# Optimization experiments

Measured on AMD Instinct MI355X. Metric: run time of the kernel, lower is better.

Reference implementation:

```python
import jax, jax.numpy as jnp
import numpy as np

NUM_HEADS = 16

def setup_inputs() -> dict:
    key = jax.random.key(0)
    kq, kk, kv = jax.random.split(key, 3)
    B, S, E = 4, 2048, 1024
    Q = jax.random.normal(kq, (B, S, E), dtype=jnp.float32)
    K = jax.random.normal(kk, (B, S, E), dtype=jnp.float32)
    V = jax.random.normal(kv, (B, S, E), dtype=jnp.float32)
    return {"Q": Q, "K": K, "V": V}

def reference(Q, K, V):
    B, S, E = Q.shape
    H = NUM_HEADS
    d_k = E // H
    # [B, H, S, d_k]
    q = Q.reshape(B, S, H, d_k).transpose(0, 2, 1, 3)
    k = K.reshape(B, S, H, d_k).transpose(0, 2, 1, 3)
    v = V.reshape(B, S, H, d_k).transpose(0, 2, 1, 3)
    scale = 1.0 / np.sqrt(d_k).astype(np.float32)
    # [B, H, S, S] full score matrix (naive attention, as in the original)
    scores = jnp.einsum('bhqd,bhkd->bhqk', q, k) * scale
    causal_mask = jnp.tril(jnp.ones((S, S), dtype=bool))
    scores = jnp.where(causal_mask, scores, jnp.finfo(scores.dtype).min)
    attn = jax.nn.softmax(scores, axis=-1)
    out = jnp.einsum('bhqk,bhkd->bhqd', attn, v)
    return out.transpose(0, 2, 1, 3).reshape(B, S, E)
```

## Files before the change

### kernel.cpp

```cpp
#include <hip/hip_runtime.h>
#include <hip/hip_bf16.h>

namespace {

constexpr int NUM_HEADS = 16;
constexpr int DK   = 64;
constexpr int SEQ  = 2048;
constexpr int EMB  = 1024;
constexpr int BR   = 128;
constexpr int BC   = 64;
constexpr int PSTR = 76;
constexpr int TILE_BYTES = 64 * 64 * 2;
constexpr float QSCALE = 0.18033688011112042f;

using frag_ab = __attribute__((ext_vector_type(8))) short;
using frag_cd = __attribute__((ext_vector_type(4))) float;

__device__ inline short f2bf(float f) {
  unsigned int u = __float_as_uint(f);
  u += 0x7fffu + ((u >> 16) & 1u);
  return (short)(u >> 16);
}

__device__ inline unsigned int pk_bf16(float a, float b) {
#if __has_builtin(__builtin_amdgcn_cvt_pk_bf16_f32)
  typedef __attribute__((ext_vector_type(2))) __bf16 bf16x2;
  bf16x2 r = __builtin_amdgcn_cvt_pk_bf16_f32(a, b);
  unsigned int u;
  __builtin_memcpy(&u, &r, 4);
  return u;
#else
  return (unsigned int)(unsigned short)f2bf(a) |
         ((unsigned int)(unsigned short)f2bf(b) << 16);
#endif
}

__device__ inline float fast_exp2(float x) {
#if __has_builtin(__builtin_amdgcn_exp2f)
  return __builtin_amdgcn_exp2f(x);
#else
  return exp2f(x);
#endif
}

__device__ __forceinline__ void gld_lds16(const void* gsrc, void* ldst) {
  __builtin_amdgcn_global_load_lds(
      (const __attribute__((address_space(1))) unsigned int*)gsrc,
      (__attribute__((address_space(3))) unsigned int*)ldst, 16, 0, 0);
}

__global__ __launch_bounds__(256)
void fa_prep(const float* __restrict__ K, const float* __restrict__ V,
             char* __restrict__ Kw, char* __restrict__ Vw)
{
  const int tid  = threadIdx.x;
  const int bh   = blockIdx.x >> 5;
  const int tile = blockIdx.x & 31;
  const int b = bh / NUM_HEADS, h = bh % NUM_HEADS;
  const float* Kb = K + (size_t)b * SEQ * EMB + h * DK;
  const float* Vb = V + (size_t)b * SEQ * EMB + h * DK;
  char* kt = Kw + ((size_t)bh * 32 + tile) * TILE_BYTES;
  char* vt = Vw + ((size_t)bh * 32 + tile) * TILE_BYTES;

#pragma unroll
  for (int i = 0; i < 2; ++i) {
    const int w = tid + i * 256;
    const int row = w >> 3, cd = w & 7;
    const float* src = Kb + (size_t)(tile * 64 + row) * EMB + cd * 8;
    const float4 a  = *(const float4*)src;
    const float4 b4 = *(const float4*)(src + 4);
    uint4 o;
    o.x = pk_bf16(a.x, a.y);  o.y = pk_bf16(a.z, a.w);
    o.z = pk_bf16(b4.x, b4.y); o.w = pk_bf16(b4.z, b4.w);
    *(uint4*)(kt + row * 128 + ((cd ^ (row & 7)) * 16)) = o;
  }
#pragma unroll
  for (int i = 0; i < 2; ++i) {
    const int w = tid + i * 256;
    const int d = w & 63, kc = w >> 6;
    float v[8];
#pragma unroll
    for (int j = 0; j < 8; ++j)
      v[j] = Vb[(size_t)(tile * 64 + kc * 8 + j) * EMB + d];
    uint4 o;
    o.x = pk_bf16(v[0], v[1]); o.y = pk_bf16(v[2], v[3]);
    o.z = pk_bf16(v[4], v[5]); o.w = pk_bf16(v[6], v[7]);
    *(uint4*)(vt + d * 128 + ((kc ^ (d & 7)) * 16)) = o;
  }
}

__global__ __launch_bounds__(256)
void fa_fwd(const float* __restrict__ Q, const char* __restrict__ Kw,
            const char* __restrict__ Vw, float* __restrict__ O)
{
  const int tid  = threadIdx.x;
  const int wave = tid >> 6;
  const int lane = tid & 63;
  const int m    = lane & 15;
  const int quad = lane >> 4;
  const int mm7  = m & 7;

  constexpr int numQ  = SEQ / BR;
  constexpr int pairs = numQ / 2;
  const int bh = blockIdx.x / pairs;
  const int p  = blockIdx.x % pairs;
  const int b  = bh / NUM_HEADS;
  const int h  = bh % NUM_HEADS;

  const float* Qb = Q + (size_t)b * SEQ * EMB + h * DK;
  float*       Ob = O + (size_t)b * SEQ * EMB + h * DK;
  const char* KwT = Kw + (size_t)bh * 32 * TILE_BYTES;
  const char* VwT = Vw + (size_t)bh * 32 * TILE_BYTES;

  __shared__ __align__(16) short Kl[64 * 64];
  __shared__ __align__(16) short Vt[64 * 64];
  __shared__ __align__(16) float Pf[4][16 * PSTR];

  const char* sbase = (wave < 2 ? KwT : VwT);
  short*      dbase = (wave < 2 ? Kl : Vt) + (wave & 1) * 2048;
  const int   shalf = (wave & 1) * 4096;

  frag_ab ones;
#pragma unroll
  for (int j = 0; j < 8; ++j) ones[j] = (short)0x3F80;

  for (int t = 0; t < 2; ++t) {
    const int qt = t ? p : (numQ - 1 - p);
    const int q0 = qt * BR;
    const int row0w = q0 + wave * 32;

    frag_ab qf[2][2];
#pragma unroll
    for (int mt = 0; mt < 2; ++mt) {
      const int qrow = row0w + mt * 16 + m;
      const float* qp = Qb + (size_t)qrow * EMB + quad * 8;
#pragma unroll
      for (int c = 0; c < 2; ++c) {
        const float4 a  = *(const float4*)(qp + c * 32);
        const float4 b4 = *(const float4*)(qp + c * 32 + 4);
        union { frag_ab f; unsigned int u[4]; } pk;
        pk.u[0] = pk_bf16(a.x * QSCALE, a.y * QSCALE);
        pk.u[1] = pk_bf16(a.z * QSCALE, a.w * QSCALE);
        pk.u[2] = pk_bf16(b4.x * QSCALE, b4.y * QSCALE);
        pk.u[3] = pk_bf16(b4.z * QSCALE, b4.w * QSCALE);
        qf[mt][c] = pk.f;
      }
    }

    frag_cd acc_o[2][4];
    frag_cd acc_l[2];
#pragma unroll
    for (int mt = 0; mt < 2; ++mt) {
      acc_l[mt] = frag_cd{0.f, 0.f, 0.f, 0.f};
#pragma unroll
      for (int n = 0; n < 4; ++n) acc_o[mt][n] = frag_cd{0.f, 0.f, 0.f, 0.f};
    }

    const int nIter = 2 * (qt + 1);
    for (int it = 0; it < nIter; ++it) {
      const int kbase = it * BC;

      __syncthreads();
      {
        const char* src = sbase + (size_t)it * TILE_BYTES + shalf + lane * 16;
#pragma unroll
        for (int j = 0; j < 4; ++j)
          gld_lds16(src + j * 1024, (char*)dbase + j * 1024);
      }
      __syncthreads();

      frag_cd s[2][4];
#pragma unroll
      for (int mt = 0; mt < 2; ++mt)
#pragma unroll
        for (int n = 0; n < 4; ++n) s[mt][n] = frag_cd{0.f, 0.f, 0.f, 0.f};
#pragma unroll
      for (int n = 0; n < 4; ++n) {
#pragma unroll
        for (int c = 0; c < 2; ++c) {
          frag_ab kf = *(const frag_ab*)(&Kl[(n * 16 + m) * 64 + (((c * 4 + quad) ^ mm7) * 8)]);
#pragma unroll
          for (int mt = 0; mt < 2; ++mt)
            s[mt][n] = __builtin_amdgcn_mfma_f32_16x16x32_bf16(qf[mt][c], kf, s[mt][n], 0, 0, 0);
        }
      }

#pragma unroll
      for (int mt = 0; mt < 2; ++mt) {
        const int row0 = row0w + mt * 16;
        if (kbase + BC > row0) {
#pragma unroll
          for (int n = 0; n < 4; ++n) {
            const int kcol = kbase + n * 16 + m;
#pragma unroll
            for (int r = 0; r < 4; ++r) {
              const int qr = row0 + quad * 4 + r;
              if (kcol > qr) s[mt][n][r] = -1e30f;
            }
          }
        }
      }

#pragma unroll
      for (int mt = 0; mt < 2; ++mt)
#pragma unroll
        for (int n = 0; n < 4; ++n)
#pragma unroll
          for (int r = 0; r < 4; ++r)
            s[mt][n][r] = fast_exp2(s[mt][n][r]);

      frag_ab vf[4][2];
#pragma unroll
      for (int n = 0; n < 4; ++n)
#pragma unroll
        for (int c = 0; c < 2; ++c)
          vf[n][c] = *(const frag_ab*)(&Vt[(n * 16 + m) * 64 + (((c * 4 + quad) ^ mm7) * 8)]);

#pragma unroll
      for (int mt = 0; mt < 2; ++mt) {
#pragma unroll
        for (int n = 0; n < 4; ++n)
#pragma unroll
          for (int r = 0; r < 4; ++r)
            Pf[wave][(quad * 4 + r) * PSTR + n * 16 + m] = s[mt][n][r];

#pragma unroll
        for (int c = 0; c < 2; ++c) {
          const float* pr = &Pf[wave][m * PSTR + c * 32 + quad * 8];
          const float4 p0 = *(const float4*)pr;
          const float4 p1 = *(const float4*)(pr + 4);
          union { frag_ab f; unsigned int u[4]; } pk;
          pk.u[0] = pk_bf16(p0.x, p0.y);
          pk.u[1] = pk_bf16(p0.z, p0.w);
          pk.u[2] = pk_bf16(p1.x, p1.y);
          pk.u[3] = pk_bf16(p1.z, p1.w);
#pragma unroll
          for (int n = 0; n < 4; ++n)
            acc_o[mt][n] = __builtin_amdgcn_mfma_f32_16x16x32_bf16(pk.f, vf[n][c], acc_o[mt][n], 0, 0, 0);
          acc_l[mt] = __builtin_amdgcn_mfma_f32_16x16x32_bf16(pk.f, ones, acc_l[mt], 0, 0, 0);
        }
      }
    }

#pragma unroll
    for (int mt = 0; mt < 2; ++mt)
#pragma unroll
      for (int r = 0; r < 4; ++r) {
        const float inv = 1.0f / acc_l[mt][r];
        const int qr = row0w + mt * 16 + quad * 4 + r;
        float* op = Ob + (size_t)qr * EMB;
#pragma unroll
        for (int n = 0; n < 4; ++n)
          op[n * 16 + m] = acc_o[mt][n][r] * inv;
      }
  }
}

__global__ __launch_bounds__(256)
void fa_fwd_fb(const float* __restrict__ Q, const float* __restrict__ K,
               const float* __restrict__ V, float* __restrict__ O)
{
  constexpr int FBR = 64, FBC = 64, FLSTR = 72;
  const int tid  = threadIdx.x;
  const int wave = tid >> 6;
  const int lane = tid & 63;
  const int m    = lane & 15;
  const int quad = lane >> 4;

  constexpr int numQ  = SEQ / FBR;
  constexpr int pairs = numQ / 2;
  const int bh = blockIdx.x / pairs;
  const int p  = blockIdx.x % pairs;
  const int b  = bh / NUM_HEADS;
  const int h  = bh % NUM_HEADS;

  const float* Qb = Q + (size_t)b * SEQ * EMB + h * DK;
  const float* Kb = K + (size_t)b * SEQ * EMB + h * DK;
  const float* Vb = V + (size_t)b * SEQ * EMB + h * DK;
  float*       Ob = O + (size_t)b * SEQ * EMB + h * DK;

  __shared__ __align__(16) short Kl[FBC * FLSTR];
  __shared__ __align__(16) short Vt[DK * FLSTR];
  __shared__ __align__(16) float Pf[4][16 * PSTR];

  for (int t = 0; t < 2; ++t) {
    const int qt = t ? p : (numQ - 1 - p);
    const int q0 = qt * FBR;

    frag_ab qf[2];
    {
      const int qrow = q0 + wave * 16 + m;
      const float* qp = Qb + (size_t)qrow * EMB + quad * 8;
#pragma unroll
      for (int c = 0; c < 2; ++c) {
        const float4 a  = *(const float4*)(qp + c * 32);
        const float4 b4 = *(const float4*)(qp + c * 32 + 4);
        union { frag_ab f; unsigned int u[4]; } pk;
        pk.u[0] = pk_bf16(a.x * QSCALE, a.y * QSCALE);
        pk.u[1] = pk_bf16(a.z * QSCALE, a.w * QSCALE);
        pk.u[2] = pk_bf16(b4.x * QSCALE, b4.y * QSCALE);
        pk.u[3] = pk_bf16(b4.z * QSCALE, b4.w * QSCALE);
        qf[c] = pk.f;
      }
    }

    float l_r[4] = {0.f, 0.f, 0.f, 0.f};
    frag_cd acc_o[4];
#pragma unroll
    for (int n = 0; n < 4; ++n) acc_o[n] = frag_cd{0.f, 0.f, 0.f, 0.f};

    const int nIter = qt + 1;
    for (int it = 0; it < nIter; ++it) {
      const int kbase = it * FBC;
      __syncthreads();
#pragma unroll
      for (int i = 0; i < 4; ++i) {
        const int idx = tid + i * 256;
        const int row = idx >> 4;
        const int c4  = (idx & 15) << 2;
        const float4 kv = *(const float4*)(Kb + (size_t)(kbase + row) * EMB + c4);
        uint2 ks;
        ks.x = pk_bf16(kv.x, kv.y);
        ks.y = pk_bf16(kv.z, kv.w);
        *(uint2*)(&Kl[row * FLSTR + c4]) = ks;
      }
#pragma unroll
      for (int i = 0; i < 2; ++i) {
        const int w    = tid + i * 256;
        const int rowp = w >> 4;
        const int c4   = (w & 15) << 2;
        const float* vp = Vb + (size_t)(kbase + 2 * rowp) * EMB + c4;
        const float4 v0 = *(const float4*)(vp);
        const float4 v1 = *(const float4*)(vp + EMB);
        *(unsigned int*)(&Vt[(c4 + 0) * FLSTR + 2 * rowp]) = pk_bf16(v0.x, v1.x);
        *(unsigned int*)(&Vt[(c4 + 1) * FLSTR + 2 * rowp]) = pk_bf16(v0.y, v1.y);
        *(unsigned int*)(&Vt[(c4 + 2) * FLSTR + 2 * rowp]) = pk_bf16(v0.z, v1.z);
        *(unsigned int*)(&Vt[(c4 + 3) * FLSTR + 2 * rowp]) = pk_bf16(v0.w, v1.w);
      }
      __syncthreads();

      frag_cd s[4];
#pragma unroll
      for (int n = 0; n < 4; ++n) {
        frag_cd a = frag_cd{0.f, 0.f, 0.f, 0.f};
#pragma unroll
        for (int c = 0; c < 2; ++c) {
          frag_ab kf = *(const frag_ab*)(&Kl[(n * 16 + m) * FLSTR + c * 32 + quad * 8]);
          a = __builtin_amdgcn_mfma_f32_16x16x32_bf16(qf[c], kf, a, 0, 0, 0);
        }
        s[n] = a;
      }
      if (kbase + FBC > q0) {
#pragma unroll
        for (int n = 0; n < 4; ++n) {
          const int kcol = kbase + n * 16 + m;
#pragma unroll
          for (int r = 0; r < 4; ++r) {
            const int qr = q0 + wave * 16 + quad * 4 + r;
            if (kcol > qr) s[n][r] = -1e30f;
          }
        }
      }
#pragma unroll
      for (int n = 0; n < 4; ++n)
#pragma unroll
        for (int r = 0; r < 4; ++r)
          s[n][r] = fast_exp2(s[n][r]);
#pragma unroll
      for (int r = 0; r < 4; ++r) {
        float rs = (s[0][r] + s[1][r]) + (s[2][r] + s[3][r]);
        rs += __shfl_xor(rs, 1);
        rs += __shfl_xor(rs, 2);
        rs += __shfl_xor(rs, 4);
        rs += __shfl_xor(rs, 8);
        l_r[r] += rs;
      }
#pragma unroll
      for (int n = 0; n < 4; ++n)
#pragma unroll
        for (int r = 0; r < 4; ++r)
          Pf[wave][(quad * 4 + r) * PSTR + n * 16 + m] = s[n][r];
#pragma unroll
      for (int c = 0; c < 2; ++c) {
        const float* pr = &Pf[wave][m * PSTR + c * 32 + quad * 8];
        const float4 p0 = *(const float4*)pr;
        const float4 p1 = *(const float4*)(pr + 4);
        union { frag_ab f; unsigned int u[4]; } pk;
        pk.u[0] = pk_bf16(p0.x, p0.y);
        pk.u[1] = pk_bf16(p0.z, p0.w);
        pk.u[2] = pk_bf16(p1.x, p1.y);
        pk.u[3] = pk_bf16(p1.z, p1.w);
#pragma unroll
        for (int n = 0; n < 4; ++n) {
          frag_ab vf = *(const frag_ab*)(&Vt[(n * 16 + m) * FLSTR + c * 32 + quad * 8]);
          acc_o[n] = __builtin_amdgcn_mfma_f32_16x16x32_bf16(pk.f, vf, acc_o[n], 0, 0, 0);
        }
      }
    }
#pragma unroll
    for (int r = 0; r < 4; ++r) {
      const float inv = 1.0f / l_r[r];
      const int qr = q0 + wave * 16 + quad * 4 + r;
      float* op = Ob + (size_t)qr * EMB;
#pragma unroll
      for (int n = 0; n < 4; ++n)
        op[n * 16 + m] = acc_o[n][r] * inv;
    }
  }
}

}

extern "C" void kernel_launch(void* const* d_in, const int* in_sizes, int n_in,
                              void* d_out, int out_size, void* d_ws, size_t ws_size,
                              hipStream_t stream) {
  const float* Q = (const float*)d_in[0];
  const float* K = (const float*)d_in[1];
  const float* V = (const float*)d_in[2];
  float* O = (float*)d_out;
  const int B = in_sizes[0] / (SEQ * EMB);
  const size_t kw_bytes = (size_t)B * NUM_HEADS * 32 * TILE_BYTES;

  if (ws_size >= 2 * kw_bytes) {
    char* Kw = (char*)d_ws;
    char* Vw = Kw + kw_bytes;
    fa_prep<<<B * NUM_HEADS * 32, 256, 0, stream>>>(K, V, Kw, Vw);
    fa_fwd<<<B * NUM_HEADS * (SEQ / BR / 2), 256, 0, stream>>>(Q, Kw, Vw, O);
  } else {
    fa_fwd_fb<<<B * NUM_HEADS * 16, 256, 0, stream>>>(Q, K, V, O);
  }
}
```

Baseline: 212.4 us.

## Double-buffer K/V tiles and launch one block per query tile

The kernel now keeps two LDS buffers for K and V and issues the async load of the next tile before computing on the current one, replacing two barriers per iteration with one. The paired-tile scheme, where each block handled a long and a short causal row block, is dropped. Instead there is one block per 128-row query tile, with heavy tiles scheduled first. Each wave also skips whole iterations that fall entirely above its causal diagonal. This doubles LDS usage and may reduce occupancy, and the grid doubles with unbalanced per-block work.

```diff
diff --git a/kernel.cpp b/kernel.cpp
--- a/kernel.cpp
+++ b/kernel.cpp
@@ -100,75 +100,81 @@
   const int quad = lane >> 4;
   const int mm7  = m & 7;
 
-  constexpr int numQ  = SEQ / BR;
-  constexpr int pairs = numQ / 2;
-  const int bh = blockIdx.x / pairs;
-  const int p  = blockIdx.x % pairs;
+  constexpr int numQ = SEQ / BR;
+  const int bh = blockIdx.x >> 4;
+  const int qt = (numQ - 1) - (blockIdx.x & 15);
   const int b  = bh / NUM_HEADS;
   const int h  = bh % NUM_HEADS;
+  const int q0 = qt * BR;
+  const int row0w = q0 + wave * 32;
 
   const float* Qb = Q + (size_t)b * SEQ * EMB + h * DK;
   float*       Ob = O + (size_t)b * SEQ * EMB + h * DK;
   const char* KwT = Kw + (size_t)bh * 32 * TILE_BYTES;
   const char* VwT = Vw + (size_t)bh * 32 * TILE_BYTES;
 
-  __shared__ __align__(16) short Kl[64 * 64];
-  __shared__ __align__(16) short Vt[64 * 64];
+  __shared__ __align__(16) short Kl[2][64 * 64];
+  __shared__ __align__(16) short Vt[2][64 * 64];
   __shared__ __align__(16) float Pf[4][16 * PSTR];
 
   const char* sbase = (wave < 2 ? KwT : VwT);
-  short*      dbase = (wave < 2 ? Kl : Vt) + (wave & 1) * 2048;
   const int   shalf = (wave & 1) * 4096;
 
   frag_ab ones;
 #pragma unroll
   for (int j = 0; j < 8; ++j) ones[j] = (short)0x3F80;
 
-  for (int t = 0; t < 2; ++t) {
-    const int qt = t ? p : (numQ - 1 - p);
-    const int q0 = qt * BR;
-    const int row0w = q0 + wave * 32;
-
-    frag_ab qf[2][2];
-#pragma unroll
-    for (int mt = 0; mt < 2; ++mt) {
-      const int qrow = row0w + mt * 16 + m;
-      const float* qp = Qb + (size_t)qrow * EMB + quad * 8;
-#pragma unroll
-      for (int c = 0; c < 2; ++c) {
-        const float4 a  = *(const float4*)(qp + c * 32);
-        const float4 b4 = *(const float4*)(qp + c * 32 + 4);
-        union { frag_ab f; unsigned int u[4]; } pk;
-        pk.u[0] = pk_bf16(a.x * QSCALE, a.y * QSCALE);
-        pk.u[1] = pk_bf16(a.z * QSCALE, a.w * QSCALE);
-        pk.u[2] = pk_bf16(b4.x * QSCALE, b4.y * QSCALE);
-        pk.u[3] = pk_bf16(b4.z * QSCALE, b4.w * QSCALE);
-        qf[mt][c] = pk.f;
-      }
-    }
-
-    frag_cd acc_o[2][4];
-    frag_cd acc_l[2];
-#pragma unroll
-    for (int mt = 0; mt < 2; ++mt) {
-      acc_l[mt] = frag_cd{0.f, 0.f, 0.f, 0.f};
-#pragma unroll
-      for (int n = 0; n < 4; ++n) acc_o[mt][n] = frag_cd{0.f, 0.f, 0.f, 0.f};
-    }
-
-    const int nIter = 2 * (qt + 1);
-    for (int it = 0; it < nIter; ++it) {
-      const int kbase = it * BC;
-
-      __syncthreads();
-      {
-        const char* src = sbase + (size_t)it * TILE_BYTES + shalf + lane * 16;
-#pragma unroll
-        for (int j = 0; j < 4; ++j)
-          gld_lds16(src + j * 1024, (char*)dbase + j * 1024);
-      }
-      __syncthreads();
-
+  frag_ab qf[2][2];
+#pragma unroll
+  for (int mt = 0; mt < 2; ++mt) {
+    const int qrow = row0w + mt * 16 + m;
+    const float* qp = Qb + (size_t)qrow * EMB + quad * 8;
+#pragma unroll
+    for (int c = 0; c < 2; ++c) {
+      const float4 a  = *(const float4*)(qp + c * 32);
+      const float4 b4 = *(const float4*)(qp + c * 32 + 4);
+      union { frag_ab f; unsigned int u[4]; } pk;
+      pk.u[0] = pk_bf16(a.x * QSCALE, a.y * QSCALE);
+      pk.u[1] = pk_bf16(a.z * QSCALE, a.w * QSCALE);
+      pk.u[2] = pk_bf16(b4.x * QSCALE, b4.y * QSCALE);
+      pk.u[3] = pk_bf16(b4.z * QSCALE, b4.w * QSCALE);
+      qf[mt][c] = pk.f;
+    }
+  }
+
+  frag_cd acc_o[2][4];
+  frag_cd acc_l[2];
+#pragma unroll
+  for (int mt = 0; mt < 2; ++mt) {
+    acc_l[mt] = frag_cd{0.f, 0.f, 0.f, 0.f};
+#pragma unroll
+    for (int n = 0; n < 4; ++n) acc_o[mt][n] = frag_cd{0.f, 0.f, 0.f, 0.f};
+  }
+
+  const int nIter = 2 * (qt + 1);
+
+  {
+    char* dst = (char*)(wave < 2 ? &Kl[0][0] : &Vt[0][0]) + shalf;
+    const char* src = sbase + shalf + lane * 16;
+#pragma unroll
+    for (int j = 0; j < 4; ++j)
+      gld_lds16(src + j * 1024, dst + j * 1024);
+  }
+  __syncthreads();
+
+  for (int it = 0; it < nIter; ++it) {
+    const int buf   = it & 1;
+    const int kbase = it * BC;
+
+    if (it + 1 < nIter) {
+      char* dst = (char*)(wave < 2 ? &Kl[buf ^ 1][0] : &Vt[buf ^ 1][0]) + shalf;
+      const char* src = sbase + (size_t)(it + 1) * TILE_BYTES + shalf + lane * 16;
+#pragma unroll
+      for (int j = 0; j < 4; ++j)
+        gld_lds16(src + j * 1024, dst + j * 1024);
+    }
+
+    if (kbase <= row0w + 31) {
       frag_cd s[2][4];
 #pragma unroll
       for (int mt = 0; mt < 2; ++mt)
@@ -178,7 +184,7 @@
       for (int n = 0; n < 4; ++n) {
 #pragma unroll
         for (int c = 0; c < 2; ++c) {
-          frag_ab kf = *(const frag_ab*)(&Kl[(n * 16 + m) * 64 + (((c * 4 + quad) ^ mm7) * 8)]);
+          frag_ab kf = *(const frag_ab*)(&Kl[buf][(n * 16 + m) * 64 + (((c * 4 + quad) ^ mm7) * 8)]);
 #pragma unroll
           for (int mt = 0; mt < 2; ++mt)
             s[mt][n] = __builtin_amdgcn_mfma_f32_16x16x32_bf16(qf[mt][c], kf, s[mt][n], 0, 0, 0);
@@ -214,7 +220,7 @@
       for (int n = 0; n < 4; ++n)
 #pragma unroll
         for (int c = 0; c < 2; ++c)
-          vf[n][c] = *(const frag_ab*)(&Vt[(n * 16 + m) * 64 + (((c * 4 + quad) ^ mm7) * 8)]);
+          vf[n][c] = *(const frag_ab*)(&Vt[buf][(n * 16 + m) * 64 + (((c * 4 + quad) ^ mm7) * 8)]);
 
 #pragma unroll
       for (int mt = 0; mt < 2; ++mt) {
@@ -242,18 +248,20 @@
       }
     }
 
-#pragma unroll
-    for (int mt = 0; mt < 2; ++mt)
-#pragma unroll
-      for (int r = 0; r < 4; ++r) {
-        const float inv = 1.0f / acc_l[mt][r];
-        const int qr = row0w + mt * 16 + quad * 4 + r;
-        float* op = Ob + (size_t)qr * EMB;
-#pragma unroll
-        for (int n = 0; n < 4; ++n)
-          op[n * 16 + m] = acc_o[mt][n][r] * inv;
-      }
-  }
+    __syncthreads();
+  }
+
+#pragma unroll
+  for (int mt = 0; mt < 2; ++mt)
+#pragma unroll
+    for (int r = 0; r < 4; ++r) {
+      const float inv = 1.0f / acc_l[mt][r];
+      const int qr = row0w + mt * 16 + quad * 4 + r;
+      float* op = Ob + (size_t)qr * EMB;
+#pragma unroll
+      for (int n = 0; n < 4; ++n)
+        op[n * 16 + m] = acc_o[mt][n][r] * inv;
+    }
 }
 
 __global__ __launch_bounds__(256)
@@ -425,7 +433,7 @@
     char* Kw = (char*)d_ws;
     char* Vw = Kw + kw_bytes;
     fa_prep<<<B * NUM_HEADS * 32, 256, 0, stream>>>(K, V, Kw, Vw);
-    fa_fwd<<<B * NUM_HEADS * (SEQ / BR / 2), 256, 0, stream>>>(Q, Kw, Vw, O);
+    fa_fwd<<<B * NUM_HEADS * (SEQ / BR), 256, 0, stream>>>(Q, Kw, Vw, O);
   } else {
     fa_fwd_fb<<<B * NUM_HEADS * 16, 256, 0, stream>>>(Q, K, V, O);
   }
```

Result: slower. 239.5 us (+12.8%).

## Split causal attention KV work evenly across blocks with partial-sum combine kernel

Applied to the files above, without the earlier changes.

Replaces the paired-query-tile forward kernel with a split-KV scheme. Each of 16 blocks per head processes exactly 17 of the 272 causal KV tile-steps, flattened across query tiles. Query tiles that straddle block boundaries write partial unnormalized outputs (bf16) and row sums to workspace, and a new combine kernel sums and normalizes them. It also skips fully masked KV tiles per wave, changes the P scratch stride, and sets an occupancy hint. This aims at load balance and double the block count, at the cost of an extra launch, extra workspace traffic, and bf16 rounding of partial accumulators.

```diff
diff --git a/kernel.cpp b/kernel.cpp
--- a/kernel.cpp
+++ b/kernel.cpp
@@ -9,8 +9,9 @@
 constexpr int EMB  = 1024;
 constexpr int BR   = 128;
 constexpr int BC   = 64;
-constexpr int PSTR = 76;
+constexpr int PSTR = 68;
 constexpr int TILE_BYTES = 64 * 64 * 2;
+constexpr int SLOT_BYTES = 128 * 64 * 2 + 128 * 4;
 constexpr float QSCALE = 0.18033688011112042f;
 
 using frag_ab = __attribute__((ext_vector_type(8))) short;
@@ -48,6 +49,8 @@
       (const __attribute__((address_space(1))) unsigned int*)gsrc,
       (__attribute__((address_space(3))) unsigned int*)ldst, 16, 0, 0);
 }
+
+__device__ __forceinline__ int tile_prefix(int qt) { return 270 - qt * qt - 3 * qt; }
 
 __global__ __launch_bounds__(256)
 void fa_prep(const float* __restrict__ K, const float* __restrict__ V,
@@ -89,9 +92,10 @@
   }
 }
 
-__global__ __launch_bounds__(256)
-void fa_fwd(const float* __restrict__ Q, const char* __restrict__ Kw,
-            const char* __restrict__ Vw, float* __restrict__ O)
+__global__ __launch_bounds__(256, 4)
+void fa_split(const float* __restrict__ Q, const char* __restrict__ Kw,
+              const char* __restrict__ Vw, float* __restrict__ O,
+              char* __restrict__ Pw)
 {
   const int tid  = threadIdx.x;
   const int wave = tid >> 6;
@@ -100,6 +104,249 @@
   const int quad = lane >> 4;
   const int mm7  = m & 7;
 
+  const int bh = blockIdx.x >> 4;
+  const int jB = blockIdx.x & 15;
+  const int b  = bh / NUM_HEADS;
+  const int h  = bh % NUM_HEADS;
+
+  const float* Qb = Q + (size_t)b * SEQ * EMB + h * DK;
+  float*       Ob = O + (size_t)b * SEQ * EMB + h * DK;
+  const char* KwT = Kw + (size_t)bh * 32 * TILE_BYTES;
+  const char* VwT = Vw + (size_t)bh * 32 * TILE_BYTES;
+
+  __shared__ __align__(16) short Kl[64 * 64];
+  __shared__ __align__(16) short Vt[64 * 64];
+  __shared__ __align__(16) float Pf[4][16 * PSTR];
+
+  const char* sbase = (wave < 2 ? KwT : VwT);
+  short*      dbase = (wave < 2 ? Kl : Vt) + (wave & 1) * 2048;
+  const int   shalf = (wave & 1) * 4096;
+
+  frag_ab ones;
+#pragma unroll
+  for (int j = 0; j < 8; ++j) ones[j] = (short)0x3F80;
+
+  const int ustart = 17 * jB;
+  const int uend   = ustart + 17;
+  int u = ustart;
+
+  while (u < uend) {
+    int qt = 0, a = 270;
+    for (int q = 15; q >= 0; --q) {
+      const int aq = tile_prefix(q);
+      if (u >= aq && u < aq + 2 * (q + 1)) { qt = q; a = aq; break; }
+    }
+    const int bEnd   = a + 2 * (qt + 1);
+    const int segEnd = (bEnd < uend) ? bEnd : uend;
+    const bool complete = (u == a) && (segEnd == bEnd);
+    const int q0 = qt * BR;
+    const int row0w = q0 + wave * 32;
+
+    frag_ab qf[2][2];
+#pragma unroll
+    for (int mt = 0; mt < 2; ++mt) {
+      const int qrow = row0w + mt * 16 + m;
+      const float* qp = Qb + (size_t)qrow * EMB + quad * 8;
+#pragma unroll
+      for (int c = 0; c < 2; ++c) {
+        const float4 a4 = *(const float4*)(qp + c * 32);
+        const float4 b4 = *(const float4*)(qp + c * 32 + 4);
+        union { frag_ab f; unsigned int uu[4]; } pk;
+        pk.uu[0] = pk_bf16(a4.x * QSCALE, a4.y * QSCALE);
+        pk.uu[1] = pk_bf16(a4.z * QSCALE, a4.w * QSCALE);
+        pk.uu[2] = pk_bf16(b4.x * QSCALE, b4.y * QSCALE);
+        pk.uu[3] = pk_bf16(b4.z * QSCALE, b4.w * QSCALE);
+        qf[mt][c] = pk.f;
+      }
+    }
+
+    frag_cd acc_o[2][4];
+    frag_cd acc_l[2];
+#pragma unroll
+    for (int mt = 0; mt < 2; ++mt) {
+      acc_l[mt] = frag_cd{0.f, 0.f, 0.f, 0.f};
+#pragma unroll
+      for (int n = 0; n < 4; ++n) acc_o[mt][n] = frag_cd{0.f, 0.f, 0.f, 0.f};
+    }
+
+    for (int it = u - a; it < segEnd - a; ++it) {
+      const int kbase = it * BC;
+
+      __syncthreads();
+      {
+        const char* src = sbase + (size_t)it * TILE_BYTES + shalf + lane * 16;
+#pragma unroll
+        for (int j = 0; j < 4; ++j)
+          gld_lds16(src + j * 1024, (char*)dbase + j * 1024);
+      }
+      __syncthreads();
+
+      if (kbase > row0w + 31) continue;
+
+      frag_cd s[2][4];
+#pragma unroll
+      for (int mt = 0; mt < 2; ++mt)
+#pragma unroll
+        for (int n = 0; n < 4; ++n) s[mt][n] = frag_cd{0.f, 0.f, 0.f, 0.f};
+#pragma unroll
+      for (int n = 0; n < 4; ++n) {
+#pragma unroll
+        for (int c = 0; c < 2; ++c) {
+          frag_ab kf = *(const frag_ab*)(&Kl[(n * 16 + m) * 64 + (((c * 4 + quad) ^ mm7) * 8)]);
+#pragma unroll
+          for (int mt = 0; mt < 2; ++mt)
+            s[mt][n] = __builtin_amdgcn_mfma_f32_16x16x32_bf16(qf[mt][c], kf, s[mt][n], 0, 0, 0);
+        }
+      }
+
+#pragma unroll
+      for (int mt = 0; mt < 2; ++mt) {
+        const int row0 = row0w + mt * 16;
+        if (kbase + BC > row0) {
+#pragma unroll
+          for (int n = 0; n < 4; ++n) {
+            const int kcol = kbase + n * 16 + m;
+#pragma unroll
+            for (int r = 0; r < 4; ++r) {
+              const int qr = row0 + quad * 4 + r;
+              if (kcol > qr) s[mt][n][r] = -1e30f;
+            }
+          }
+        }
+      }
+
+#pragma unroll
+      for (int mt = 0; mt < 2; ++mt)
+#pragma unroll
+        for (int n = 0; n < 4; ++n)
+#pragma unroll
+          for (int r = 0; r < 4; ++r)
+            s[mt][n][r] = fast_exp2(s[mt][n][r]);
+
+      frag_ab vf[4][2];
+#pragma unroll
+      for (int n = 0; n < 4; ++n)
+#pragma unroll
+        for (int c = 0; c < 2; ++c)
+          vf[n][c] = *(const frag_ab*)(&Vt[(n * 16 + m) * 64 + (((c * 4 + quad) ^ mm7) * 8)]);
+
+#pragma unroll
+      for (int mt = 0; mt < 2; ++mt) {
+#pragma unroll
+        for (int n = 0; n < 4; ++n)
+#pragma unroll
+          for (int r = 0; r < 4; ++r)
+            Pf[wave][(quad * 4 + r) * PSTR + n * 16 + m] = s[mt][n][r];
+
+#pragma unroll
+        for (int c = 0; c < 2; ++c) {
+          const float* pr = &Pf[wave][m * PSTR + c * 32 + quad * 8];
+          const float4 p0 = *(const float4*)pr;
+          const float4 p1 = *(const float4*)(pr + 4);
+          union { frag_ab f; unsigned int uu[4]; } pk;
+          pk.uu[0] = pk_bf16(p0.x, p0.y);
+          pk.uu[1] = pk_bf16(p0.z, p0.w);
+          pk.uu[2] = pk_bf16(p1.x, p1.y);
+          pk.uu[3] = pk_bf16(p1.z, p1.w);
+#pragma unroll
+          for (int n = 0; n < 4; ++n)
+            acc_o[mt][n] = __builtin_amdgcn_mfma_f32_16x16x32_bf16(pk.f, vf[n][c], acc_o[mt][n], 0, 0, 0);
+          acc_l[mt] = __builtin_amdgcn_mfma_f32_16x16x32_bf16(pk.f, ones, acc_l[mt], 0, 0, 0);
+        }
+      }
+    }
+
+    if (complete) {
+#pragma unroll
+      for (int mt = 0; mt < 2; ++mt)
+#pragma unroll
+        for (int r = 0; r < 4; ++r) {
+          const float inv = 1.0f / acc_l[mt][r];
+          const int qr = row0w + mt * 16 + quad * 4 + r;
+          float* op = Ob + (size_t)qr * EMB;
+#pragma unroll
+          for (int n = 0; n < 4; ++n)
+            op[n * 16 + m] = acc_o[mt][n][r] * inv;
+        }
+    } else {
+      const int role = (u == ustart) ? 0 : 1;
+      char* slot = Pw + ((size_t)blockIdx.x * 2 + role) * SLOT_BYTES;
+      short* sn = (short*)slot;
+      float* sl = (float*)(slot + 128 * 64 * 2);
+#pragma unroll
+      for (int mt = 0; mt < 2; ++mt)
+#pragma unroll
+        for (int r = 0; r < 4; ++r) {
+          const int row = wave * 32 + mt * 16 + quad * 4 + r;
+#pragma unroll
+          for (int n = 0; n < 4; ++n)
+            sn[row * 64 + n * 16 + m] = f2bf(acc_o[mt][n][r]);
+          if (m == 0) sl[row] = acc_l[mt][r];
+        }
+    }
+
+    u = segEnd;
+  }
+}
+
+__global__ __launch_bounds__(256)
+void fa_combine(float* __restrict__ O, const char* __restrict__ Pw)
+{
+  const int bh = blockIdx.x / 15;
+  const int jb = (blockIdx.x % 15) + 1;
+  const int u  = 17 * jb;
+
+  int qt = 0, a = 270;
+  for (int q = 15; q >= 0; --q) {
+    const int aq = tile_prefix(q);
+    if (u >= aq && u < aq + 2 * (q + 1)) { qt = q; a = aq; break; }
+  }
+  const int bEnd = a + 2 * (qt + 1);
+  if (a >= u) return;
+  if (jb != a / 17 + 1) return;
+
+  const int b = bh / NUM_HEADS, h = bh % NUM_HEADS;
+  const int row = threadIdx.x >> 1;
+  const int c0  = (threadIdx.x & 1) * 32;
+
+  float acc[32];
+#pragma unroll
+  for (int c = 0; c < 32; ++c) acc[c] = 0.f;
+  float lsum = 0.f;
+
+  const int jlo = a / 17, jhi = (bEnd - 1) / 17;
+  for (int jj = jlo; jj <= jhi; ++jj) {
+    const int role = (a <= 17 * jj) ? 0 : 1;
+    const char* slot = Pw + (((size_t)bh * 16 + jj) * 2 + role) * SLOT_BYTES;
+    const short* sn = (const short*)slot;
+    const float* sl = (const float*)(slot + 128 * 64 * 2);
+    lsum += sl[row];
+    const short* rp = sn + row * 64 + c0;
+#pragma unroll
+    for (int c = 0; c < 32; ++c) {
+      const unsigned int us = (unsigned short)rp[c];
+      acc[c] += __uint_as_float(us << 16);
+    }
+  }
+
+  const float inv = 1.0f / lsum;
+  const int qrow = qt * BR + row;
+  float* op = O + (size_t)b * SEQ * EMB + (size_t)qrow * EMB + h * DK + c0;
+#pragma unroll
+  for (int c = 0; c < 32; ++c) op[c] = acc[c] * inv;
+}
+
+__global__ __launch_bounds__(256)
+void fa_paired(const float* __restrict__ Q, const char* __restrict__ Kw,
+               const char* __restrict__ Vw, float* __restrict__ O)
+{
+  const int tid  = threadIdx.x;
+  const int wave = tid >> 6;
+  const int lane = tid & 63;
+  const int m    = lane & 15;
+  const int quad = lane >> 4;
+  const int mm7  = m & 7;
+
   constexpr int numQ  = SEQ / BR;
   constexpr int pairs = numQ / 2;
   const int bh = blockIdx.x / pairs;
@@ -136,13 +383,13 @@
       const float* qp = Qb + (size_t)qrow * EMB + quad * 8;
 #pragma unroll
       for (int c = 0; c < 2; ++c) {
-        const float4 a  = *(const float4*)(qp + c * 32);
+        const float4 a4 = *(const float4*)(qp + c * 32);
         const float4 b4 = *(const float4*)(qp + c * 32 + 4);
-        union { frag_ab f; unsigned int u[4]; } pk;
-        pk.u[0] = pk_bf16(a.x * QSCALE, a.y * QSCALE);
-        pk.u[1] = pk_bf16(a.z * QSCALE, a.w * QSCALE);
-        pk.u[2] = pk_bf16(b4.x * QSCALE, b4.y * QSCALE);
-        pk.u[3] = pk_bf16(b4.z * QSCALE, b4.w * QSCALE);
+        union { frag_ab f; unsigned int uu[4]; } pk;
+        pk.uu[0] = pk_bf16(a4.x * QSCALE, a4.y * QSCALE);
+        pk.uu[1] = pk_bf16(a4.z * QSCALE, a4.w * QSCALE);
+        pk.uu[2] = pk_bf16(b4.x * QSCALE, b4.y * QSCALE);
+        pk.uu[3] = pk_bf16(b4.z * QSCALE, b4.w * QSCALE);
         qf[mt][c] = pk.f;
       }
     }
@@ -159,7 +406,6 @@
     const int nIter = 2 * (qt + 1);
     for (int it = 0; it < nIter; ++it) {
       const int kbase = it * BC;
-
       __syncthreads();
       {
         const char* src = sbase + (size_t)it * TILE_BYTES + shalf + lane * 16;
@@ -168,6 +414,7 @@
           gld_lds16(src + j * 1024, (char*)dbase + j * 1024);
       }
       __syncthreads();
+      if (kbase > row0w + 31) continue;
 
       frag_cd s[2][4];
 #pragma unroll
@@ -184,7 +431,6 @@
             s[mt][n] = __builtin_amdgcn_mfma_f32_16x16x32_bf16(qf[mt][c], kf, s[mt][n], 0, 0, 0);
         }
       }
-
 #pragma unroll
       for (int mt = 0; mt < 2; ++mt) {
         const int row0 = row0w + mt * 16;
@@ -200,7 +446,6 @@
           }
         }
       }
-
 #pragma unroll
       for (int mt = 0; mt < 2; ++mt)
 #pragma unroll
@@ -223,17 +468,16 @@
 #pragma unroll
           for (int r = 0; r < 4; ++r)
             Pf[wave][(quad * 4 + r) * PSTR + n * 16 + m] = s[mt][n][r];
-
 #pragma unroll
         for (int c = 0; c < 2; ++c) {
           const float* pr = &Pf[wave][m * PSTR + c * 32 + quad * 8];
           const float4 p0 = *(const float4*)pr;
           const float4 p1 = *(const float4*)(pr + 4);
-          union { frag_ab f; unsigned int u[4]; } pk;
-          pk.u[0] = pk_bf16(p0.x, p0.y);
-          pk.u[1] = pk_bf16(p0.z, p0.w);
-          pk.u[2] = pk_bf16(p1.x, p1.y);
-          pk.u[3] = pk_bf16(p1.z, p1.w);
+          union { frag_ab f; unsigned int uu[4]; } pk;
+          pk.uu[0] = pk_bf16(p0.x, p0.y);
+          pk.uu[1] = pk_bf16(p0.z, p0.w);
+          pk.uu[2] = pk_bf16(p1.x, p1.y);
+          pk.uu[3] = pk_bf16(p1.z, p1.w);
 #pragma unroll
           for (int n = 0; n < 4; ++n)
             acc_o[mt][n] = __builtin_amdgcn_mfma_f32_16x16x32_bf16(pk.f, vf[n][c], acc_o[mt][n], 0, 0, 0);
@@ -293,13 +537,13 @@
       const float* qp = Qb + (size_t)qrow * EMB + quad * 8;
 #pragma unroll
       for (int c = 0; c < 2; ++c) {
-        const float4 a  = *(const float4*)(qp + c * 32);
+        const float4 a4 = *(const float4*)(qp + c * 32);
         const float4 b4 = *(const float4*)(qp + c * 32 + 4);
-        union { frag_ab f; unsigned int u[4]; } pk;
-        pk.u[0] = pk_bf16(a.x * QSCALE, a.y * QSCALE);
-        pk.u[1] = pk_bf16(a.z * QSCALE, a.w * QSCALE);
-        pk.u[2] = pk_bf16(b4.x * QSCALE, b4.y * QSCALE);
-        pk.u[3] = pk_bf16(b4.z * QSCALE, b4.w * QSCALE);
+        union { frag_ab f; unsigned int uu[4]; } pk;
+        pk.uu[0] = pk_bf16(a4.x * QSCALE, a4.y * QSCALE);
+        pk.uu[1] = pk_bf16(a4.z * QSCALE, a4.w * QSCALE);
+        pk.uu[2] = pk_bf16(b4.x * QSCALE, b4.y * QSCALE);
+        pk.uu[3] = pk_bf16(b4.z * QSCALE, b4.w * QSCALE);
         qf[c] = pk.f;
       }
     }
@@ -385,11 +629,11 @@
         const float* pr = &Pf[wave][m * PSTR + c * 32 + quad * 8];
         const float4 p0 = *(const float4*)pr;
         const float4 p1 = *(const float4*)(pr + 4);
-        union { frag_ab f; unsigned int u[4]; } pk;
-        pk.u[0] = pk_bf16(p0.x, p0.y);
-        pk.u[1] = pk_bf16(p0.z, p0.w);
-        pk.u[2] = pk_bf16(p1.x, p1.y);
-        pk.u[3] = pk_bf16(p1.z, p1.w);
+        union { frag_ab f; unsigned int uu[4]; } pk;
+        pk.uu[0] = pk_bf16(p0.x, p0.y);
+        pk.uu[1] = pk_bf16(p0.z, p0.w);
+        pk.uu[2] = pk_bf16(p1.x, p1.y);
+        pk.uu[3] = pk_bf16(p1.z, p1.w);
 #pragma unroll
         for (int n = 0; n < 4; ++n) {
           frag_ab vf = *(const frag_ab*)(&Vt[(n * 16 + m) * FLSTR + c * 32 + quad * 8]);
@@ -419,14 +663,23 @@
   const float* V = (const float*)d_in[2];
   float* O = (float*)d_out;
   const int B = in_sizes[0] / (SEQ * EMB);
-  const size_t kw_bytes = (size_t)B * NUM_HEADS * 32 * TILE_BYTES;
-
-  if (ws_size >= 2 * kw_bytes) {
+  const int BH = B * NUM_HEADS;
+  const size_t kw_bytes   = (size_t)BH * 32 * TILE_BYTES;
+  const size_t slot_bytes = (size_t)BH * 16 * 2 * SLOT_BYTES;
+
+  if (ws_size >= 2 * kw_bytes + slot_bytes) {
     char* Kw = (char*)d_ws;
     char* Vw = Kw + kw_bytes;
-    fa_prep<<<B * NUM_HEADS * 32, 256, 0, stream>>>(K, V, Kw, Vw);
-    fa_fwd<<<B * NUM_HEADS * (SEQ / BR / 2), 256, 0, stream>>>(Q, Kw, Vw, O);
+    char* Pw = Vw + kw_bytes;
+    fa_prep<<<BH * 32, 256, 0, stream>>>(K, V, Kw, Vw);
+    fa_split<<<BH * 16, 256, 0, stream>>>(Q, Kw, Vw, O, Pw);
+    fa_combine<<<BH * 15, 256, 0, stream>>>(O, Pw);
+  } else if (ws_size >= 2 * kw_bytes) {
+    char* Kw = (char*)d_ws;
+    char* Vw = Kw + kw_bytes;
+    fa_prep<<<BH * 32, 256, 0, stream>>>(K, V, Kw, Vw);
+    fa_paired<<<BH * 8, 256, 0, stream>>>(Q, Kw, Vw, O);
   } else {
-    fa_fwd_fb<<<B * NUM_HEADS * 16, 256, 0, stream>>>(Q, K, V, O);
-  }
-}
+    fa_fwd_fb<<<BH * 16, 256, 0, stream>>>(Q, K, V, O);
+  }
+}
```

Measured after the change: 251.6 us. 1.18x slower.
